# Performance work log

Measured on AMD Instinct MI355X. Metric: run time of the kernel, lower is better.

## Reference

```python
import jax, jax.numpy as jnp
import numpy as np

DIM = 96
HEADS = 4
WS = (2, 7, 7)      # window size (wd, wh, ww)
SS = (1, 3, 3)      # shift size
RES = (16, 56, 56)  # (D, H, W)
BATCH = 4
HIDDEN = 384        # mlp_ratio * dim
EPS = 1e-5


def _rel_pos_index(ws):
    wd, wh, ww = ws
    c = np.stack(np.meshgrid(np.arange(wd), np.arange(wh), np.arange(ww), indexing='ij')).reshape(3, -1)
    r = (c[:, :, None] - c[:, None, :]).transpose(1, 2, 0)  # (N, N, 3)
    r[..., 0] += wd - 1
    r[..., 1] += wh - 1
    r[..., 2] += ww - 1
    r[..., 0] *= (2 * wh - 1) * (2 * ww - 1)
    r[..., 1] *= (2 * ww - 1)
    return r.sum(-1)  # (N, N) int


def _attn_mask(res, ws, ss):
    D, H, W = res
    wd, wh, ww = ws
    sd, sh, sw = ss
    img = np.zeros((D, H, W), np.float32)
    cnt = 0
    for dsl in (slice(0, -wd), slice(-wd, -sd), slice(-sd, None)):
        for hsl in (slice(0, -wh), slice(-wh, -sh), slice(-sh, None)):
            for wsl in (slice(0, -ww), slice(-ww, -sw), slice(-sw, None)):
                img[dsl, hsl, wsl] = cnt
                cnt += 1
    N = wd * wh * ww
    m = img.reshape(D // wd, wd, H // wh, wh, W // ww, ww).transpose(0, 2, 4, 1, 3, 5).reshape(-1, N)
    am = m[:, None, :] - m[:, :, None]
    return np.where(am != 0, np.float32(-100.0), np.float32(0.0))  # (nW, N, N)


def setup_inputs() -> dict:
    key = jax.random.key(0)
    ks = jax.random.split(key, 8)
    s = 0.02
    return {
        'x': jax.random.normal(ks[0], (BATCH, DIM) + RES, jnp.float32),
        'gamma1': jnp.ones((DIM,), jnp.float32),
        'beta1': jnp.zeros((DIM,), jnp.float32),
        'gamma2': jnp.ones((DIM,), jnp.float32),
        'beta2': jnp.zeros((DIM,), jnp.float32),
        'qkv_w': jax.random.normal(ks[1], (DIM, 3 * DIM), jnp.float32) * s,
        'qkv_b': jnp.zeros((3 * DIM,), jnp.float32),
        'proj_w': jax.random.normal(ks[2], (DIM, DIM), jnp.float32) * s,
        'proj_b': jnp.zeros((DIM,), jnp.float32),
        'rpb_table': jax.random.normal(ks[3], ((2 * WS[0] - 1) * (2 * WS[1] - 1) * (2 * WS[2] - 1), HEADS), jnp.float32) * s,
        'fc1_w': jax.random.normal(ks[4], (DIM, HIDDEN), jnp.float32) * s,
        'fc1_b': jnp.zeros((HIDDEN,), jnp.float32),
        'fc2_w': jax.random.normal(ks[5], (HIDDEN, DIM), jnp.float32) * s,
        'fc2_b': jnp.zeros((DIM,), jnp.float32),
    }


def _layernorm(t, g, b):
    mu = t.mean(-1, keepdims=True)
    var = ((t - mu) ** 2).mean(-1, keepdims=True)
    return (t - mu) / jnp.sqrt(var + EPS) * g + b


def reference(x, gamma1, beta1, gamma2, beta2, qkv_w, qkv_b, proj_w, proj_b,
              rpb_table, fc1_w, fc1_b, fc2_w, fc2_b):
    B, C, D, H, W = x.shape
    wd, wh, ww = WS
    sd, sh, sw = SS
    N = wd * wh * ww
    nH = HEADS
    dh = C // nH

    rpi = jnp.asarray(_rel_pos_index(WS))          # (N, N) static
    mask = jnp.asarray(_attn_mask(RES, WS, SS))    # (nW, N, N) static
    nW = mask.shape[0]

    xl = jnp.transpose(x, (0, 2, 3, 4, 1))  # (B, D, H, W, C) channels-last

    # norm1 + cyclic shift
    h = _layernorm(xl, gamma1, beta1)
    h = jnp.roll(h, (-sd, -sh, -sw), axis=(1, 2, 3))

    # window partition -> (B*nW, N, C)
    win = h.reshape(B, D // wd, wd, H // wh, wh, W // ww, ww, C)
    win = win.transpose(0, 1, 3, 5, 2, 4, 6, 7).reshape(-1, N, C)

    # window attention
    qkv = (win @ qkv_w + qkv_b).reshape(-1, N, 3, nH, dh).transpose(2, 0, 3, 1, 4)
    q, k, v = qkv[0] * (dh ** -0.5), qkv[1], qkv[2]  # (B_, nH, N, dh)
    attn = jnp.einsum('bhnd,bhmd->bhnm', q, k)       # (B_, nH, N, N)
    rpb = rpb_table[rpi].transpose(2, 0, 1)          # (nH, N, N)
    attn = attn + rpb[None]
    attn = attn.reshape(B, nW, nH, N, N) + mask[None, :, None]
    attn = jax.nn.softmax(attn.reshape(-1, nH, N, N), axis=-1)
    out = jnp.einsum('bhnm,bhmd->bhnd', attn, v).transpose(0, 2, 1, 3).reshape(-1, N, C)
    out = out @ proj_w + proj_b

    # window reverse + reverse shift
    out = out.reshape(B, D // wd, H // wh, W // ww, wd, wh, ww, C)
    out = out.transpose(0, 1, 4, 2, 5, 3, 6, 7).reshape(B, D, H, W, C)
    out = jnp.roll(out, (sd, sh, sw), axis=(1, 2, 3))

    xl = xl + out  # residual 1

    # norm2 + 1x1-conv FFN (pointwise = matmul over channel)
    h2 = _layernorm(xl, gamma2, beta2)
    h2 = jax.nn.gelu(h2 @ fc1_w + fc1_b, approximate=False) @ fc2_w + fc2_b
    xl = xl + h2  # residual 2

    return jnp.transpose(xl, (0, 4, 1, 2, 3))  # back to (B, C, D, H, W)
```

## Files before the change

### kernel.cpp

```cpp
#include <hip/hip_runtime.h>
#include <hip/hip_bf16.h>
#include <cmath>

#define C_DIM 96
#define RES_D 16
#define RES_H 56
#define RES_W 56
#define BATCH 4
#define SPATIAL (RES_D*RES_H*RES_W)
#define NTOK (BATCH*SPATIAL)
#define NWIN_TOT 2048
#define EPS_LN 1e-5f
#define QSCALE 0.2041241452319315f

#define MPAD 112

#define OFF_P   0
#define OFF_Q   14336
#define OFF_K   28672
#define OFF_VT  43008
#define SM_TOT  59392

typedef float f32x4 __attribute__((ext_vector_type(4)));
typedef short s16x8 __attribute__((ext_vector_type(8)));
typedef unsigned u32x4 __attribute__((ext_vector_type(4)));
typedef unsigned u32x2 __attribute__((ext_vector_type(2)));
typedef unsigned short u16;

__device__ __forceinline__ u16 f2bf(float f) {
    unsigned u = __float_as_uint(f);
    u = (u + 0x7FFF + ((u >> 16) & 1)) >> 16;
    return (u16)u;
}
__device__ __forceinline__ unsigned pk2(float lo, float hi) {
    return (unsigned)f2bf(lo) | ((unsigned)f2bf(hi) << 16);
}
__device__ __forceinline__ int swzP(int r, int c) {
    return r * 128 + ((((c >> 3) ^ (r & 15)) << 3) | (c & 7));
}
__device__ __forceinline__ int swzQ(int r, int c) {
    return r * 32 + ((((c >> 3) ^ ((r >> 1) & 3)) << 3) | (c & 7));
}

__device__ __forceinline__ float wave_reduce_sum(float v) {
#pragma unroll
    for (int off = 32; off > 0; off >>= 1) v += __shfl_xor(v, off, 64);
    return v;
}

__global__ __launch_bounds__(256) void k_prep(
    const float* __restrict__ qkv_w, const float* __restrict__ proj_w,
    const float* __restrict__ fc1_w, const float* __restrict__ fc2_w,
    const float* __restrict__ rpb_table,
    u16* __restrict__ wq, u16* __restrict__ wp, u16* __restrict__ w1,
    u16* __restrict__ w2, float* __restrict__ rpbm) {
    int i = blockIdx.x * 256 + threadIdx.x;
    if (i < 27648) {
        int j = i / 96, c = i % 96;
        wq[i] = f2bf(qkv_w[c * 288 + j]);
    } else if (i < 36864) {
        int t = i - 27648; int j = t / 96, c = t % 96;
        wp[t] = f2bf(proj_w[c * 96 + j]);
    } else if (i < 73728) {
        int t = i - 36864; int j = t / 96, c = t % 96;
        w1[t] = f2bf(fc1_w[c * 384 + j]);
    } else if (i < 110592) {
        int t = i - 73728; int c = t / 384, j = t % 384;
        w2[t] = f2bf(fc2_w[j * 96 + c]);
    } else if (i < 176128) {
        int t = i - 110592;
        int h = t / 16384, r = t % 16384, n = r / 128, m = r % 128;
        float v;
        if (m >= 98) {
            v = -30000.0f;
        } else if (n >= 98) {
            v = 0.0f;
        } else {
            int dzn = n / 49, rn = n % 49, hyn = rn / 7, wxn = rn % 7;
            int dzm = m / 49, rm = m % 49, hym = rm / 7, wxm = rm % 7;
            int ridx = (dzn - dzm + 1) * 169 + (hyn - hym + 6) * 13 + (wxn - wxm + 6);
            v = rpb_table[ridx * 4 + h];
        }
        rpbm[t] = v;
    }
}

__global__ __launch_bounds__(256) void k_transpose_in(const float* __restrict__ x,
                                                      float* __restrict__ xl) {
    __shared__ float tile[32][33];
    const int b = blockIdx.z;
    const int s0 = blockIdx.x * 32;
    const int c0 = blockIdx.y * 32;
    const float* xb = x + (size_t)b * C_DIM * SPATIAL;
    float* xlb = xl + (size_t)b * SPATIAL * C_DIM;
    const int ts = threadIdx.x, tc = threadIdx.y;
#pragma unroll
    for (int i = 0; i < 32; i += 8)
        tile[tc + i][ts] = xb[(size_t)(c0 + tc + i) * SPATIAL + s0 + ts];
    __syncthreads();
#pragma unroll
    for (int i = 0; i < 32; i += 8)
        xlb[(size_t)(s0 + tc + i) * C_DIM + c0 + ts] = tile[ts][tc + i];
}

__global__ __launch_bounds__(448, 2) void k_win_attn(
    const float* __restrict__ xl, float* __restrict__ xl2,
    const float* __restrict__ g1, const float* __restrict__ b1,
    const u16* __restrict__ wqkv, const float* __restrict__ qkv_b,
    const u16* __restrict__ wproj, const float* __restrict__ proj_b,
    const float* __restrict__ rpbm) {
    __shared__ __align__(16) u16 sm[SM_TOT];
    __shared__ __align__(16) int s_gtok[MPAD];
    __shared__ __align__(16) int s_reg[MPAD];

    const int tid = threadIdx.x;
    const int lane = tid & 63;
    const int wv = tid >> 6;
    const int g4 = lane >> 4;
    const int c16 = lane & 15;
    const int mt = wv;

    const int wid = blockIdx.x;
    const int b = wid >> 9;
    const int rem = wid & 511;
    const int wdi = rem >> 6, whi = (rem >> 3) & 7, wwi = rem & 7;

    for (int i = tid; i < 7168; i += 448) {
        int c = 24 + (i & 7);
        int hb = (i >> 3) / 112;
        int r = (i >> 3) % 112;
        int base = (hb < 4) ? (OFF_Q + hb * 3584) : (OFF_K + (hb - 4) * 3584);
        sm[base + swzQ(r, c)] = 0;
    }
    for (int i = tid; i < 4096; i += 448) {
        int h = i >> 10, rr = 24 + ((i >> 7) & 7), c = i & 127;
        sm[OFF_VT + h * 4096 + swzP(rr, c)] = 0;
    }
    for (int i = tid; i < 1536; i += 448) {
        int h = i / 384, r = (i % 384) >> 4, c = 112 + (i & 15);
        sm[OFF_VT + h * 4096 + swzP(r, c)] = 0;
    }
    for (int i = tid; i < 1792; i += 448) {
        int r = i >> 4, c = 112 + (i & 15);
        sm[OFF_P + swzP(r, c)] = 0;
    }
    if (tid < MPAD) {
        if (tid < 98) {
            const int n = tid;
            const int dz = n / 49, r = n % 49, hy = r / 7, wx = r % 7;
            const int rd = wdi * 2 + dz, rh = whi * 7 + hy, rw = wwi * 7 + wx;
            int od = rd + 1; if (od >= RES_D) od -= RES_D;
            int oh = rh + 3; if (oh >= RES_H) oh -= RES_H;
            int ow = rw + 3; if (ow >= RES_W) ow -= RES_W;
            s_gtok[n] = ((b * RES_D + od) * RES_H + oh) * RES_W + ow;
            const int gd = (rd < 14) ? 0 : (rd < 15 ? 1 : 2);
            const int gh = (rh < 49) ? 0 : (rh < 53 ? 1 : 2);
            const int gw = (rw < 49) ? 0 : (rw < 53 ? 1 : 2);
            s_reg[n] = gd * 9 + gh * 3 + gw;
        } else { s_gtok[tid] = 0; s_reg[tid] = -1; }
    }
    __syncthreads();

    const int mytok = mt * 16 + c16;
    const float live = (mytok < 98) ? 1.0f : 0.0f;

    u32x4 xa[3];
    {
        const float* src = xl + (size_t)s_gtok[mytok] * C_DIM;
        f32x4 xv0 = *(const f32x4*)(src + 0 * 32 + g4 * 8);
        f32x4 xv1 = *(const f32x4*)(src + 0 * 32 + g4 * 8 + 4);
        f32x4 xv2 = *(const f32x4*)(src + 1 * 32 + g4 * 8);
        f32x4 xv3 = *(const f32x4*)(src + 1 * 32 + g4 * 8 + 4);
        f32x4 xv4 = *(const f32x4*)(src + 2 * 32 + g4 * 8);
        f32x4 xv5 = *(const f32x4*)(src + 2 * 32 + g4 * 8 + 4);
        float lsum = (xv0[0]+xv0[1]+xv0[2]+xv0[3]) + (xv1[0]+xv1[1]+xv1[2]+xv1[3])
                   + (xv2[0]+xv2[1]+xv2[2]+xv2[3]) + (xv3[0]+xv3[1]+xv3[2]+xv3[3])
                   + (xv4[0]+xv4[1]+xv4[2]+xv4[3]) + (xv5[0]+xv5[1]+xv5[2]+xv5[3]);
        lsum += __shfl_xor(lsum, 16, 64);
        lsum += __shfl_xor(lsum, 32, 64);
        const float mu = lsum * (1.0f / 96.0f);
        f32x4 d0 = xv0 - mu, d1 = xv1 - mu, d2 = xv2 - mu,
              d3 = xv3 - mu, d4 = xv4 - mu, d5 = xv5 - mu;
        float lvv = (d0[0]*d0[0]+d0[1]*d0[1]+d0[2]*d0[2]+d0[3]*d0[3])
                  + (d1[0]*d1[0]+d1[1]*d1[1]+d1[2]*d1[2]+d1[3]*d1[3])
                  + (d2[0]*d2[0]+d2[1]*d2[1]+d2[2]*d2[2]+d2[3]*d2[3])
                  + (d3[0]*d3[0]+d3[1]*d3[1]+d3[2]*d3[2]+d3[3]*d3[3])
                  + (d4[0]*d4[0]+d4[1]*d4[1]+d4[2]*d4[2]+d4[3]*d4[3])
                  + (d5[0]*d5[0]+d5[1]*d5[1]+d5[2]*d5[2]+d5[3]*d5[3]);
        lvv += __shfl_xor(lvv, 16, 64);
        lvv += __shfl_xor(lvv, 32, 64);
        const float rstd = rsqrtf(lvv * (1.0f / 96.0f) + EPS_LN) * live;
#pragma unroll
        for (int ks = 0; ks < 3; ++ks) {
            const f32x4 ea = (ks == 0) ? d0 : (ks == 1) ? d2 : d4;
            const f32x4 eb = (ks == 0) ? d1 : (ks == 1) ? d3 : d5;
            f32x4 ga = *(const f32x4*)(g1 + ks * 32 + g4 * 8);
            f32x4 gb = *(const f32x4*)(g1 + ks * 32 + g4 * 8 + 4);
            f32x4 ba = *(const f32x4*)(b1 + ks * 32 + g4 * 8);
            f32x4 bb = *(const f32x4*)(b1 + ks * 32 + g4 * 8 + 4);
            f32x4 y0 = ea * rstd * ga + ba * live;
            f32x4 y1 = eb * rstd * gb + bb * live;
            xa[ks][0] = pk2(y0[0], y0[1]);
            xa[ks][1] = pk2(y0[2], y0[3]);
            xa[ks][2] = pk2(y1[0], y1[1]);
            xa[ks][3] = pk2(y1[2], y1[3]);
        }
    }

#pragma unroll
    for (int sel = 0; sel < 3; ++sel) {
#pragma unroll
        for (int t = 0; t < 6; ++t) {
            const int nt = sel * 6 + t;
            f32x4 acc = {0.f, 0.f, 0.f, 0.f};
            if (sel < 2) {
#pragma unroll
                for (int ks = 0; ks < 3; ++ks) {
                    s16x8 bw = *(const s16x8*)(wqkv + (size_t)(nt * 16 + c16) * 96 + ks * 32 + g4 * 8);
                    acc = __builtin_amdgcn_mfma_f32_16x16x32_bf16(bw, __builtin_bit_cast(s16x8, xa[ks]), acc, 0, 0, 0);
                }
                const int jb = t * 16 + g4 * 4;
                const f32x4 b4 = *(const f32x4*)(qkv_b + sel * 96 + jb);
                f32x4 v = acc + b4;
                if (sel == 0) { v[0] *= QSCALE; v[1] *= QSCALE; v[2] *= QSCALE; v[3] *= QSCALE; }
                const int h = jb / 24, db = jb - h * 24;
                u32x2 pkv = { pk2(v[0], v[1]), pk2(v[2], v[3]) };
                const int base = (sel == 0 ? OFF_Q : OFF_K) + h * 3584;
                *(u32x2*)&sm[base + swzQ(mytok, db)] = pkv;
            } else {
#pragma unroll
                for (int ks = 0; ks < 3; ++ks) {
                    s16x8 bw = *(const s16x8*)(wqkv + (size_t)(nt * 16 + c16) * 96 + ks * 32 + g4 * 8);
                    acc = __builtin_amdgcn_mfma_f32_16x16x32_bf16(__builtin_bit_cast(s16x8, xa[ks]), bw, acc, 0, 0, 0);
                }
                const int j96 = t * 16 + c16;
                const float bias = qkv_b[192 + j96];
                const int h = j96 / 24, d = j96 - h * 24;
                const int row0 = mt * 16 + g4 * 4;
                f32x4 v = acc + bias;
                u32x2 pkv = { pk2(v[0], v[1]), pk2(v[2], v[3]) };
                *(u32x2*)&sm[OFF_VT + h * 4096 + swzP(d, row0)] = pkv;
            }
        }
    }
    __syncthreads();

    const int rgq = s_reg[mytok];
    unsigned mbits = 0;
#pragma unroll
    for (int nt = 0; nt < 7; ++nt) {
        const int4 cr = *(const int4*)&s_reg[nt * 16 + g4 * 4];
        mbits |= (unsigned)(cr.x != rgq) << (nt * 4 + 0);
        mbits |= (unsigned)(cr.y != rgq) << (nt * 4 + 1);
        mbits |= (unsigned)(cr.z != rgq) << (nt * 4 + 2);
        mbits |= (unsigned)(cr.w != rgq) << (nt * 4 + 3);
    }

    unsigned ogp[4][2][2];
#pragma unroll
    for (int h = 0; h < 4; ++h) {
        const s16x8 aq = *(const s16x8*)&sm[OFF_Q + h * 3584 + swzQ(mytok, g4 * 8)];
        const float* rq = rpbm + h * 16384 + mytok * 128;
        float smr = 0.f;
#pragma unroll
        for (int nt = 0; nt < 7; ++nt) {
            s16x8 ak = *(const s16x8*)&sm[OFF_K + h * 3584 + swzQ(nt * 16 + c16, g4 * 8)];
            f32x4 z = {0.f, 0.f, 0.f, 0.f};
            f32x4 sc = __builtin_amdgcn_mfma_f32_16x16x32_bf16(ak, aq, z, 0, 0, 0);
            const f32x4 rv = *(const f32x4*)&rq[nt * 16 + g4 * 4];
            float s0 = sc[0] + rv[0] - 100.0f * (float)((mbits >> (nt * 4 + 0)) & 1u);
            float s1 = sc[1] + rv[1] - 100.0f * (float)((mbits >> (nt * 4 + 1)) & 1u);
            float s2 = sc[2] + rv[2] - 100.0f * (float)((mbits >> (nt * 4 + 2)) & 1u);
            float s3 = sc[3] + rv[3] - 100.0f * (float)((mbits >> (nt * 4 + 3)) & 1u);
            const float e0 = __expf(s0), e1 = __expf(s1), e2 = __expf(s2), e3 = __expf(s3);
            smr += (e0 + e1) + (e2 + e3);
            u32x2 pkv = { pk2(e0, e1), pk2(e2, e3) };
            *(u32x2*)&sm[OFF_P + swzP(mytok, nt * 16 + g4 * 4)] = pkv;
        }
        smr += __shfl_xor(smr, 16, 64);
        smr += __shfl_xor(smr, 32, 64);
        const float iq = 1.0f / fmaxf(smr, 1e-30f);
#pragma unroll
        for (int dt = 0; dt < 2; ++dt) {
            f32x4 acc = {0.f, 0.f, 0.f, 0.f};
#pragma unroll
            for (int ks = 0; ks < 4; ++ks) {
                s16x8 av = *(const s16x8*)&sm[OFF_VT + h * 4096 + swzP(dt * 16 + c16, ks * 32 + g4 * 8)];
                s16x8 bp = *(const s16x8*)&sm[OFF_P + swzP(mt * 16 + c16, ks * 32 + g4 * 8)];
                acc = __builtin_amdgcn_mfma_f32_16x16x32_bf16(av, bp, acc, 0, 0, 0);
            }
            ogp[h][dt][0] = pk2(acc[0] * iq, acc[1] * iq);
            ogp[h][dt][1] = pk2(acc[2] * iq, acc[3] * iq);
        }
    }

#pragma unroll
    for (int h = 0; h < 4; ++h) {
#pragma unroll
        for (int dt = 0; dt < 2; ++dt) {
            const int db = dt * 16 + g4 * 4;
            if (db < 24) {
                u32x2 v = { ogp[h][dt][0], ogp[h][dt][1] };
                *(u32x2*)&sm[OFF_P + swzP(mytok, h * 24 + db)] = v;
            }
        }
    }

    const int gq = s_gtok[mytok];
#pragma unroll
    for (int nt = 0; nt < 6; ++nt) {
        f32x4 acc = {0.f, 0.f, 0.f, 0.f};
#pragma unroll
        for (int ks = 0; ks < 3; ++ks) {
            s16x8 aw = *(const s16x8*)(wproj + (size_t)(nt * 16 + c16) * 96 + ks * 32 + g4 * 8);
            s16x8 bo = *(const s16x8*)&sm[OFF_P + swzP(mt * 16 + c16, ks * 32 + g4 * 8)];
            acc = __builtin_amdgcn_mfma_f32_16x16x32_bf16(aw, bo, acc, 0, 0, 0);
        }
        if (mytok < 98) {
            const int cb = nt * 16 + g4 * 4;
            const f32x4 pb4 = *(const f32x4*)(proj_b + cb);
            const f32x4 res = *(const f32x4*)(xl + (size_t)gq * C_DIM + cb);
            *(f32x4*)(xl2 + (size_t)gq * C_DIM + cb) = acc + pb4 + res;
        }
    }
}

__global__ __launch_bounds__(256, 3) void k_ffn(
    const float* __restrict__ xl2, float* __restrict__ out,
    const float* __restrict__ g2, const float* __restrict__ b2,
    const u16* __restrict__ w1, const float* __restrict__ fc1_b,
    const u16* __restrict__ w2, const float* __restrict__ fc2_b) {
    __shared__ __align__(16) u16 sg[64 * 384];
    float* s_res = (float*)sg;

    const int tid = threadIdx.x;
    const int lane = tid & 63;
    const int wave = tid >> 6;
    const int g4 = lane >> 4, c16 = lane & 15;
    const int mg = wave & 1;
    const int nh = wave >> 1;
    const int t0 = blockIdx.x * 64;

    u32x4 xa[2][3];
#pragma unroll
    for (int g = 0; g < 2; ++g) {
        const int tok = mg * 32 + g * 16 + c16;
        const float* src = xl2 + (size_t)(t0 + tok) * C_DIM;
        f32x4 xv0 = *(const f32x4*)(src + 0 * 32 + g4 * 8);
        f32x4 xv1 = *(const f32x4*)(src + 0 * 32 + g4 * 8 + 4);
        f32x4 xv2 = *(const f32x4*)(src + 1 * 32 + g4 * 8);
        f32x4 xv3 = *(const f32x4*)(src + 1 * 32 + g4 * 8 + 4);
        f32x4 xv4 = *(const f32x4*)(src + 2 * 32 + g4 * 8);
        f32x4 xv5 = *(const f32x4*)(src + 2 * 32 + g4 * 8 + 4);
        float lsum = (xv0[0]+xv0[1]+xv0[2]+xv0[3]) + (xv1[0]+xv1[1]+xv1[2]+xv1[3])
                   + (xv2[0]+xv2[1]+xv2[2]+xv2[3]) + (xv3[0]+xv3[1]+xv3[2]+xv3[3])
                   + (xv4[0]+xv4[1]+xv4[2]+xv4[3]) + (xv5[0]+xv5[1]+xv5[2]+xv5[3]);
        lsum += __shfl_xor(lsum, 16, 64);
        lsum += __shfl_xor(lsum, 32, 64);
        const float mu = lsum * (1.0f / 96.0f);
        f32x4 d0 = xv0 - mu, d1 = xv1 - mu, d2 = xv2 - mu,
              d3 = xv3 - mu, d4 = xv4 - mu, d5 = xv5 - mu;
        float lvv = (d0[0]*d0[0]+d0[1]*d0[1]+d0[2]*d0[2]+d0[3]*d0[3])
                  + (d1[0]*d1[0]+d1[1]*d1[1]+d1[2]*d1[2]+d1[3]*d1[3])
                  + (d2[0]*d2[0]+d2[1]*d2[1]+d2[2]*d2[2]+d2[3]*d2[3])
                  + (d3[0]*d3[0]+d3[1]*d3[1]+d3[2]*d3[2]+d3[3]*d3[3])
                  + (d4[0]*d4[0]+d4[1]*d4[1]+d4[2]*d4[2]+d4[3]*d4[3])
                  + (d5[0]*d5[0]+d5[1]*d5[1]+d5[2]*d5[2]+d5[3]*d5[3]);
        lvv += __shfl_xor(lvv, 16, 64);
        lvv += __shfl_xor(lvv, 32, 64);
        const float rstd = rsqrtf(lvv * (1.0f / 96.0f) + EPS_LN);
#pragma unroll
        for (int ks = 0; ks < 3; ++ks) {
            const f32x4 ea = (ks == 0) ? d0 : (ks == 1) ? d2 : d4;
            const f32x4 eb = (ks == 0) ? d1 : (ks == 1) ? d3 : d5;
            f32x4 ga = *(const f32x4*)(g2 + ks * 32 + g4 * 8);
            f32x4 gb = *(const f32x4*)(g2 + ks * 32 + g4 * 8 + 4);
            f32x4 ba = *(const f32x4*)(b2 + ks * 32 + g4 * 8);
            f32x4 bb = *(const f32x4*)(b2 + ks * 32 + g4 * 8 + 4);
            f32x4 y0 = ea * rstd * ga + ba;
            f32x4 y1 = eb * rstd * gb + bb;
            xa[g][ks][0] = pk2(y0[0], y0[1]);
            xa[g][ks][1] = pk2(y0[2], y0[3]);
            xa[g][ks][2] = pk2(y1[0], y1[1]);
            xa[g][ks][3] = pk2(y1[2], y1[3]);
        }
    }

#pragma unroll 1
    for (int i = 0; i < 12; ++i) {
        const int nt = nh * 12 + i;
        f32x4 acc0 = {0.f, 0.f, 0.f, 0.f};
        f32x4 acc1 = {0.f, 0.f, 0.f, 0.f};
#pragma unroll
        for (int ks = 0; ks < 3; ++ks) {
            s16x8 aw = *(const s16x8*)(w1 + (size_t)(nt * 16 + c16) * 96 + ks * 32 + g4 * 8);
            acc0 = __builtin_amdgcn_mfma_f32_16x16x32_bf16(aw, __builtin_bit_cast(s16x8, xa[0][ks]), acc0, 0, 0, 0);
            acc1 = __builtin_amdgcn_mfma_f32_16x16x32_bf16(aw, __builtin_bit_cast(s16x8, xa[1][ks]), acc1, 0, 0, 0);
        }
        const f32x4 bias = *(const f32x4*)(fc1_b + nt * 16 + g4 * 4);
#pragma unroll
        for (int g = 0; g < 2; ++g) {
            const f32x4 acc = (g == 0) ? acc0 : acc1;
            const int tok = mg * 32 + g * 16 + c16;
            float gv[4];
#pragma unroll
            for (int r = 0; r < 4; ++r) {
                const float v = acc[r] + bias[r];
                gv[r] = 0.5f * v * (1.0f + erff(v * 0.70710678118654752f));
            }
            const int chunk = (2 * nt + (g4 >> 1)) ^ (tok & 15);
            u32x2 pk = { pk2(gv[0], gv[1]), pk2(gv[2], gv[3]) };
            *(u32x2*)&sg[tok * 384 + chunk * 8 + (g4 & 1) * 4] = pk;
        }
    }
    __syncthreads();

    f32x4 facc[3][2];
    const int tokA = mg * 32 + c16;
    const int tokB = tokA + 16;
#pragma unroll 1
    for (int i = 0; i < 3; ++i) {
        const int nt = nh * 3 + i;
        f32x4 a0 = {0.f, 0.f, 0.f, 0.f};
        f32x4 a1 = {0.f, 0.f, 0.f, 0.f};
#pragma unroll
        for (int ks = 0; ks < 12; ++ks) {
            s16x8 aw = *(const s16x8*)(w2 + (size_t)(nt * 16 + c16) * 384 + ks * 32 + g4 * 8);
            s16x8 bg0 = *(const s16x8*)&sg[tokA * 384 + (((ks * 4 + g4) ^ (tokA & 15)) << 3)];
            s16x8 bg1 = *(const s16x8*)&sg[tokB * 384 + (((ks * 4 + g4) ^ (tokB & 15)) << 3)];
            a0 = __builtin_amdgcn_mfma_f32_16x16x32_bf16(aw, bg0, a0, 0, 0, 0);
            a1 = __builtin_amdgcn_mfma_f32_16x16x32_bf16(aw, bg1, a1, 0, 0, 0);
        }
        const f32x4 bias = *(const f32x4*)(fc2_b + nt * 16 + g4 * 4);
        const f32x4 resA = *(const f32x4*)(xl2 + (size_t)(t0 + tokA) * C_DIM + nt * 16 + g4 * 4);
        const f32x4 resB = *(const f32x4*)(xl2 + (size_t)(t0 + tokB) * C_DIM + nt * 16 + g4 * 4);
        facc[i][0] = a0 + bias + resA;
        facc[i][1] = a1 + bias + resB;
    }
    __syncthreads();

#pragma unroll
    for (int i = 0; i < 3; ++i) {
        const int nt = nh * 3 + i;
#pragma unroll
        for (int g = 0; g < 2; ++g) {
            const int tok = mg * 32 + g * 16 + c16;
#pragma unroll
            for (int r = 0; r < 4; ++r)
                s_res[tok * 97 + nt * 16 + g4 * 4 + r] = facc[i][g][r];
        }
    }
    __syncthreads();

    const int bb = t0 / SPATIAL;
    const int sbase = t0 % SPATIAL;
    for (int e = tid; e < 1536; e += 256) {
        const int c = e >> 4, tq = e & 15;
        f32x4 v;
        v[0] = s_res[(tq * 4 + 0) * 97 + c];
        v[1] = s_res[(tq * 4 + 1) * 97 + c];
        v[2] = s_res[(tq * 4 + 2) * 97 + c];
        v[3] = s_res[(tq * 4 + 3) * 97 + c];
        *(f32x4*)&out[((size_t)bb * C_DIM + c) * SPATIAL + sbase + tq * 4] = v;
    }
}

extern "C" void kernel_launch(void* const* d_in, const int* in_sizes, int n_in,
                              void* d_out, int out_size, void* d_ws, size_t ws_size,
                              hipStream_t stream) {
    const float* x      = (const float*)d_in[0];
    const float* g1     = (const float*)d_in[1];
    const float* be1    = (const float*)d_in[2];
    const float* g2     = (const float*)d_in[3];
    const float* be2    = (const float*)d_in[4];
    const float* qkv_w  = (const float*)d_in[5];
    const float* qkv_b  = (const float*)d_in[6];
    const float* proj_w = (const float*)d_in[7];
    const float* proj_b = (const float*)d_in[8];
    const float* rpb    = (const float*)d_in[9];
    const float* fc1_w  = (const float*)d_in[10];
    const float* fc1_b  = (const float*)d_in[11];
    const float* fc2_w  = (const float*)d_in[12];
    const float* fc2_b  = (const float*)d_in[13];
    float* out = (float*)d_out;

    float* xl  = (float*)d_ws;
    float* xl2 = xl + (size_t)NTOK * C_DIM;
    u16* wq = (u16*)(xl2 + (size_t)NTOK * C_DIM);
    u16* wp = wq + 27648;
    u16* w1 = wp + 9216;
    u16* w2 = w1 + 36864;
    float* rpbm = (float*)(w2 + 36864);

    k_prep<<<688, 256, 0, stream>>>(qkv_w, proj_w, fc1_w, fc2_w, rpb, wq, wp, w1, w2, rpbm);
    k_transpose_in<<<dim3(SPATIAL / 32, C_DIM / 32, BATCH), dim3(32, 8), 0, stream>>>(x, xl);
    k_win_attn<<<NWIN_TOT, 448, 0, stream>>>(xl, xl2, g1, be1, wq, qkv_b, wp, proj_b, rpbm);
    k_ffn<<<NTOK / 64, 256, 0, stream>>>(xl2, out, g2, be2, w1, fc1_b, w2, fc2_b);
}
```

Baseline: 354.4 us.

## Process attention heads in two pairs to halve Q/K/V shared memory

Restructures the QKV projection and attention so that two heads at a time are projected into shared memory and attended, in two passes. This cuts the Q, K and V^T staging buffers in half, reducing LDS per block and likely allowing more blocks per CU for latency hiding. It adds extra barriers and splits the projection loop into two phases, which adds some synchronization cost.

```diff
diff --git a/kernel.cpp b/kernel.cpp
--- a/kernel.cpp
+++ b/kernel.cpp
@@ -17,9 +17,9 @@
 
 #define OFF_P   0
 #define OFF_Q   14336
-#define OFF_K   28672
-#define OFF_VT  43008
-#define SM_TOT  59392
+#define OFF_K   21504
+#define OFF_VT  28672
+#define SM_TOT  36864
 
 typedef float f32x4 __attribute__((ext_vector_type(4)));
 typedef short s16x8 __attribute__((ext_vector_type(8)));
@@ -125,18 +125,18 @@
     const int rem = wid & 511;
     const int wdi = rem >> 6, whi = (rem >> 3) & 7, wwi = rem & 7;
 
-    for (int i = tid; i < 7168; i += 448) {
+    for (int i = tid; i < 3584; i += 448) {
         int c = 24 + (i & 7);
-        int hb = (i >> 3) / 112;
+        int slab = (i >> 3) / 112;
         int r = (i >> 3) % 112;
-        int base = (hb < 4) ? (OFF_Q + hb * 3584) : (OFF_K + (hb - 4) * 3584);
+        int base = (slab < 2) ? (OFF_Q + slab * 3584) : (OFF_K + (slab - 2) * 3584);
         sm[base + swzQ(r, c)] = 0;
     }
-    for (int i = tid; i < 4096; i += 448) {
+    for (int i = tid; i < 2048; i += 448) {
         int h = i >> 10, rr = 24 + ((i >> 7) & 7), c = i & 127;
         sm[OFF_VT + h * 4096 + swzP(rr, c)] = 0;
     }
-    for (int i = tid; i < 1536; i += 448) {
+    for (int i = tid; i < 768; i += 448) {
         int h = i / 384, r = (i % 384) >> 4, c = 112 + (i & 15);
         sm[OFF_VT + h * 4096 + swzP(r, c)] = 0;
     }
@@ -207,44 +207,6 @@
         }
     }
 
-#pragma unroll
-    for (int sel = 0; sel < 3; ++sel) {
-#pragma unroll
-        for (int t = 0; t < 6; ++t) {
-            const int nt = sel * 6 + t;
-            f32x4 acc = {0.f, 0.f, 0.f, 0.f};
-            if (sel < 2) {
-#pragma unroll
-                for (int ks = 0; ks < 3; ++ks) {
-                    s16x8 bw = *(const s16x8*)(wqkv + (size_t)(nt * 16 + c16) * 96 + ks * 32 + g4 * 8);
-                    acc = __builtin_amdgcn_mfma_f32_16x16x32_bf16(bw, __builtin_bit_cast(s16x8, xa[ks]), acc, 0, 0, 0);
-                }
-                const int jb = t * 16 + g4 * 4;
-                const f32x4 b4 = *(const f32x4*)(qkv_b + sel * 96 + jb);
-                f32x4 v = acc + b4;
-                if (sel == 0) { v[0] *= QSCALE; v[1] *= QSCALE; v[2] *= QSCALE; v[3] *= QSCALE; }
-                const int h = jb / 24, db = jb - h * 24;
-                u32x2 pkv = { pk2(v[0], v[1]), pk2(v[2], v[3]) };
-                const int base = (sel == 0 ? OFF_Q : OFF_K) + h * 3584;
-                *(u32x2*)&sm[base + swzQ(mytok, db)] = pkv;
-            } else {
-#pragma unroll
-                for (int ks = 0; ks < 3; ++ks) {
-                    s16x8 bw = *(const s16x8*)(wqkv + (size_t)(nt * 16 + c16) * 96 + ks * 32 + g4 * 8);
-                    acc = __builtin_amdgcn_mfma_f32_16x16x32_bf16(__builtin_bit_cast(s16x8, xa[ks]), bw, acc, 0, 0, 0);
-                }
-                const int j96 = t * 16 + c16;
-                const float bias = qkv_b[192 + j96];
-                const int h = j96 / 24, d = j96 - h * 24;
-                const int row0 = mt * 16 + g4 * 4;
-                f32x4 v = acc + bias;
-                u32x2 pkv = { pk2(v[0], v[1]), pk2(v[2], v[3]) };
-                *(u32x2*)&sm[OFF_VT + h * 4096 + swzP(d, row0)] = pkv;
-            }
-        }
-    }
-    __syncthreads();
-
     const int rgq = s_reg[mytok];
     unsigned mbits = 0;
 #pragma unroll
@@ -258,40 +220,83 @@
 
     unsigned ogp[4][2][2];
 #pragma unroll
-    for (int h = 0; h < 4; ++h) {
-        const s16x8 aq = *(const s16x8*)&sm[OFF_Q + h * 3584 + swzQ(mytok, g4 * 8)];
-        const float* rq = rpbm + h * 16384 + mytok * 128;
-        float smr = 0.f;
-#pragma unroll
-        for (int nt = 0; nt < 7; ++nt) {
-            s16x8 ak = *(const s16x8*)&sm[OFF_K + h * 3584 + swzQ(nt * 16 + c16, g4 * 8)];
-            f32x4 z = {0.f, 0.f, 0.f, 0.f};
-            f32x4 sc = __builtin_amdgcn_mfma_f32_16x16x32_bf16(ak, aq, z, 0, 0, 0);
-            const f32x4 rv = *(const f32x4*)&rq[nt * 16 + g4 * 4];
-            float s0 = sc[0] + rv[0] - 100.0f * (float)((mbits >> (nt * 4 + 0)) & 1u);
-            float s1 = sc[1] + rv[1] - 100.0f * (float)((mbits >> (nt * 4 + 1)) & 1u);
-            float s2 = sc[2] + rv[2] - 100.0f * (float)((mbits >> (nt * 4 + 2)) & 1u);
-            float s3 = sc[3] + rv[3] - 100.0f * (float)((mbits >> (nt * 4 + 3)) & 1u);
-            const float e0 = __expf(s0), e1 = __expf(s1), e2 = __expf(s2), e3 = __expf(s3);
-            smr += (e0 + e1) + (e2 + e3);
-            u32x2 pkv = { pk2(e0, e1), pk2(e2, e3) };
-            *(u32x2*)&sm[OFF_P + swzP(mytok, nt * 16 + g4 * 4)] = pkv;
-        }
-        smr += __shfl_xor(smr, 16, 64);
-        smr += __shfl_xor(smr, 32, 64);
-        const float iq = 1.0f / fmaxf(smr, 1e-30f);
-#pragma unroll
-        for (int dt = 0; dt < 2; ++dt) {
-            f32x4 acc = {0.f, 0.f, 0.f, 0.f};
-#pragma unroll
-            for (int ks = 0; ks < 4; ++ks) {
-                s16x8 av = *(const s16x8*)&sm[OFF_VT + h * 4096 + swzP(dt * 16 + c16, ks * 32 + g4 * 8)];
-                s16x8 bp = *(const s16x8*)&sm[OFF_P + swzP(mt * 16 + c16, ks * 32 + g4 * 8)];
-                acc = __builtin_amdgcn_mfma_f32_16x16x32_bf16(av, bp, acc, 0, 0, 0);
+    for (int p = 0; p < 2; ++p) {
+#pragma unroll
+        for (int sel = 0; sel < 3; ++sel) {
+#pragma unroll
+            for (int t = 0; t < 3; ++t) {
+                const int nt = sel * 6 + p * 3 + t;
+                f32x4 acc = {0.f, 0.f, 0.f, 0.f};
+                if (sel < 2) {
+#pragma unroll
+                    for (int ks = 0; ks < 3; ++ks) {
+                        s16x8 bw = *(const s16x8*)(wqkv + (size_t)(nt * 16 + c16) * 96 + ks * 32 + g4 * 8);
+                        acc = __builtin_amdgcn_mfma_f32_16x16x32_bf16(bw, __builtin_bit_cast(s16x8, xa[ks]), acc, 0, 0, 0);
+                    }
+                    const int lt = t * 16 + g4 * 4;
+                    const f32x4 b4 = *(const f32x4*)(qkv_b + sel * 96 + p * 48 + lt);
+                    f32x4 v = acc + b4;
+                    if (sel == 0) { v[0] *= QSCALE; v[1] *= QSCALE; v[2] *= QSCALE; v[3] *= QSCALE; }
+                    const int hp = lt / 24, db = lt - hp * 24;
+                    u32x2 pkv = { pk2(v[0], v[1]), pk2(v[2], v[3]) };
+                    const int base = (sel == 0 ? OFF_Q : OFF_K) + hp * 3584;
+                    *(u32x2*)&sm[base + swzQ(mytok, db)] = pkv;
+                } else {
+#pragma unroll
+                    for (int ks = 0; ks < 3; ++ks) {
+                        s16x8 bw = *(const s16x8*)(wqkv + (size_t)(nt * 16 + c16) * 96 + ks * 32 + g4 * 8);
+                        acc = __builtin_amdgcn_mfma_f32_16x16x32_bf16(__builtin_bit_cast(s16x8, xa[ks]), bw, acc, 0, 0, 0);
+                    }
+                    const int lj = t * 16 + c16;
+                    const float bias = qkv_b[192 + p * 48 + lj];
+                    const int hp = lj / 24, d = lj - hp * 24;
+                    const int row0 = mt * 16 + g4 * 4;
+                    f32x4 v = acc + bias;
+                    u32x2 pkv = { pk2(v[0], v[1]), pk2(v[2], v[3]) };
+                    *(u32x2*)&sm[OFF_VT + hp * 4096 + swzP(d, row0)] = pkv;
+                }
             }
-            ogp[h][dt][0] = pk2(acc[0] * iq, acc[1] * iq);
-            ogp[h][dt][1] = pk2(acc[2] * iq, acc[3] * iq);
-        }
+        }
+        __syncthreads();
+
+#pragma unroll
+        for (int hp = 0; hp < 2; ++hp) {
+            const int h = p * 2 + hp;
+            const s16x8 aq = *(const s16x8*)&sm[OFF_Q + hp * 3584 + swzQ(mytok, g4 * 8)];
+            const float* rq = rpbm + h * 16384 + mytok * 128;
+            float smr = 0.f;
+#pragma unroll
+            for (int nt = 0; nt < 7; ++nt) {
+                s16x8 ak = *(const s16x8*)&sm[OFF_K + hp * 3584 + swzQ(nt * 16 + c16, g4 * 8)];
+                f32x4 z = {0.f, 0.f, 0.f, 0.f};
+                f32x4 sc = __builtin_amdgcn_mfma_f32_16x16x32_bf16(ak, aq, z, 0, 0, 0);
+                const f32x4 rv = *(const f32x4*)&rq[nt * 16 + g4 * 4];
+                float s0 = sc[0] + rv[0] - 100.0f * (float)((mbits >> (nt * 4 + 0)) & 1u);
+                float s1 = sc[1] + rv[1] - 100.0f * (float)((mbits >> (nt * 4 + 1)) & 1u);
+                float s2 = sc[2] + rv[2] - 100.0f * (float)((mbits >> (nt * 4 + 2)) & 1u);
+                float s3 = sc[3] + rv[3] - 100.0f * (float)((mbits >> (nt * 4 + 3)) & 1u);
+                const float e0 = __expf(s0), e1 = __expf(s1), e2 = __expf(s2), e3 = __expf(s3);
+                smr += (e0 + e1) + (e2 + e3);
+                u32x2 pkv = { pk2(e0, e1), pk2(e2, e3) };
+                *(u32x2*)&sm[OFF_P + swzP(mytok, nt * 16 + g4 * 4)] = pkv;
+            }
+            smr += __shfl_xor(smr, 16, 64);
+            smr += __shfl_xor(smr, 32, 64);
+            const float iq = 1.0f / fmaxf(smr, 1e-30f);
+#pragma unroll
+            for (int dt = 0; dt < 2; ++dt) {
+                f32x4 acc = {0.f, 0.f, 0.f, 0.f};
+#pragma unroll
+                for (int ks = 0; ks < 4; ++ks) {
+                    s16x8 av = *(const s16x8*)&sm[OFF_VT + hp * 4096 + swzP(dt * 16 + c16, ks * 32 + g4 * 8)];
+                    s16x8 bp = *(const s16x8*)&sm[OFF_P + swzP(mt * 16 + c16, ks * 32 + g4 * 8)];
+                    acc = __builtin_amdgcn_mfma_f32_16x16x32_bf16(av, bp, acc, 0, 0, 0);
+                }
+                ogp[h][dt][0] = pk2(acc[0] * iq, acc[1] * iq);
+                ogp[h][dt][1] = pk2(acc[2] * iq, acc[3] * iq);
+            }
+        }
+        if (p == 0) __syncthreads();
     }
 
 #pragma unroll
```

New measurement: 416.8 us. 17.6% more time.
